# Kernel optimization log

Hardware: AMD Instinct MI355X
Metric: run time of the kernel (lower is better)

Reference implementation:

```python
import jax, jax.numpy as jnp
import numpy as np
import math

B, S, D, E, H = 8, 384, 768, 768, 12
HD = E // H
MAXL = 512

def _xavier(key, shape):
    fan_in, fan_out = shape[1], shape[0]
    lim = math.sqrt(6.0 / (fan_in + fan_out))
    return jax.random.uniform(key, shape, jnp.float32, -lim, lim)

def setup_inputs() -> dict:
    key = jax.random.key(0)
    ks = jax.random.split(key, 12)
    return {
        "x": jax.random.normal(ks[0], (B, S, D), jnp.float32),
        "mask": jnp.ones((B, S), jnp.int32),
        "segment_ids": jax.random.randint(ks[1], (B, S), 0, 2).astype(jnp.int32),
        "sep_distances": jax.random.normal(ks[2], (B, S), jnp.float32),
        "Wq": _xavier(ks[3], (E, D)), "bq": jnp.zeros((E,), jnp.float32),
        "Wk": _xavier(ks[4], (E, D)), "bk": jnp.zeros((E,), jnp.float32),
        "Wv": _xavier(ks[5], (E, D)), "bv": jnp.zeros((E,), jnp.float32),
        "rel_emb": jax.random.normal(ks[6], (2 * MAXL - 1, D), jnp.float32),
        "Wpk": _xavier(ks[7], (E, D)), "bpk": jnp.zeros((E,), jnp.float32),
        "Wpq": _xavier(ks[8], (E, D)), "bpq": jnp.zeros((E,), jnp.float32),
        "same_bias": jnp.zeros((H,), jnp.float32),
        "cross_bias": jnp.zeros((H,), jnp.float32),
        "sep_scale": jnp.full((H,), 0.25, jnp.float32),
        "sep_decay": jnp.full((H,), 0.35, jnp.float32),
        "Wo": _xavier(ks[9], (D, E)), "bo": jnp.zeros((D,), jnp.float32),
    }

def reference(x, mask, segment_ids, sep_distances, Wq, bq, Wk, bk, Wv, bv,
              rel_emb, Wpk, bpk, Wpq, bpq, same_bias, cross_bias,
              sep_scale, sep_decay, Wo, bo):
    b, s, _ = x.shape
    def shape_heads(t):  # [b,s,E] -> [b,H,s,HD]
        return t.reshape(b, s, H, HD).transpose(0, 2, 1, 3)
    q = shape_heads(x @ Wq.T + bq)
    k = shape_heads(x @ Wk.T + bk)
    v = shape_heads(x @ Wv.T + bv)
    # relative positions i - j, clamped and shifted
    rel_pos = jnp.arange(s)[:, None] - jnp.arange(s)[None, :]
    rel_pos = jnp.clip(rel_pos, -(MAXL - 1), MAXL - 1) + (MAXL - 1)
    rel = rel_emb[rel_pos]                     # [s,s,D]
    pos_k = (rel @ Wpk.T + bpk).reshape(s, s, H, HD)  # [i,j,h,d]
    pos_q = (rel @ Wpq.T + bpq).reshape(s, s, H, HD)
    c2c = jnp.einsum('bhid,bhjd->bhij', q, k)
    c2p = jnp.einsum('bhid,ijhd->bhij', q, pos_k)
    p2c = jnp.einsum('ijhd,bhjd->bhij', pos_q, k)
    logits = (c2c + c2p + p2c) / math.sqrt(HD * 3.0)
    # segment bias
    same = (segment_ids[:, :, None] == segment_ids[:, None, :]).astype(jnp.float32)[:, None]  # [b,1,s,s]
    cross = 1.0 - same
    hb = lambda p: p[None, :, None, None]
    seg_bias = same * hb(same_bias) + cross * hb(cross_bias)
    abs_sep = jnp.abs(sep_distances)
    gap = jnp.abs(abs_sep[:, :, None] - abs_sep[:, None, :])[:, None]  # [b,1,s,s]
    decay = jax.nn.softplus(sep_decay)[None, :, None, None] + 1e-4
    seg_bias = seg_bias + cross * jnp.exp(-gap * decay) * hb(sep_scale)
    logits = logits + seg_bias
    # mask: [b,s] -> [b,1,1,s]
    m = mask[:, None, None, :]
    logits = jnp.where(m == 0, jnp.float32(-9e15), logits)
    attn = jax.nn.softmax(logits, axis=-1)
    vals = jnp.einsum('bhij,bhjd->bhid', attn, v)
    vals = vals.transpose(0, 2, 1, 3).reshape(b, s, E)
    return vals @ Wo.T + bo
```

## Files before the change

kernel.cpp:

```cpp
#include <hip/hip_runtime.h>
#include <math.h>

#define B_  8
#define S_  384
#define H_  12
#define HD_ 64
#define E_  768
#define D_  768

typedef float  floatx4 __attribute__((ext_vector_type(4)));
typedef __bf16 bf16x8  __attribute__((ext_vector_type(8)));
typedef unsigned int ux4 __attribute__((ext_vector_type(4)));

__device__ __forceinline__ unsigned short f2bf(float f) {
    union { float f; unsigned u; } x; x.f = f;
    unsigned r = x.u + 0x7fff + ((x.u >> 16) & 1);
    return (unsigned short)(r >> 16);
}
__device__ __forceinline__ float bf2f(unsigned short u) {
    union { unsigned u; float f; } x; x.u = ((unsigned)u) << 16;
    return x.f;
}
__device__ __forceinline__ bf16x8 gld8(const unsigned short* p) {
    return __builtin_bit_cast(bf16x8, *(const ux4*)p);
}
__device__ __forceinline__ int tadr(int row, int cD) {
    return (row * 8 + (cD ^ (row & 7))) * 8;
}
__device__ __forceinline__ bf16x8 lds8(const unsigned short* base, int row, int cD) {
    return __builtin_bit_cast(bf16x8, *(const ux4*)(base + tadr(row, cD)));
}

__global__ __launch_bounds__(256) void convert_all(
    const float* __restrict__ x,
    const float* __restrict__ Wq, const float* __restrict__ Wk,
    const float* __restrict__ Wv, const float* __restrict__ Wo,
    const float* __restrict__ Wpk, const float* __restrict__ Wpq,
    const float* __restrict__ rel128,
    unsigned short* __restrict__ xb,
    unsigned short* __restrict__ wqb, unsigned short* __restrict__ wkb,
    unsigned short* __restrict__ wvb, unsigned short* __restrict__ wob,
    unsigned short* __restrict__ wpkb, unsigned short* __restrict__ wpqb,
    unsigned short* __restrict__ relb)
{
    const int seg = blockIdx.y;
    const int e = (blockIdx.x * 256 + threadIdx.x) * 4;
    const float* src;
    unsigned short* dst;
    if (seg < 4)       { src = x + (size_t)seg * 589824; dst = xb + (size_t)seg * 589824; }
    else if (seg == 4) { src = Wq;  dst = wqb; }
    else if (seg == 5) { src = Wk;  dst = wkb; }
    else if (seg == 6) { src = Wv;  dst = wvb; }
    else if (seg == 7) { src = Wo;  dst = wob; }
    else if (seg == 8) { src = Wpk; dst = wpkb; }
    else if (seg == 9) { src = Wpq; dst = wpqb; }
    else               { src = rel128; dst = relb; }

    float4 v;
    if (seg == 10 && e >= 767 * 768) v = make_float4(0.f, 0.f, 0.f, 0.f);
    else                             v = *(const float4*)(src + e);
    ushort4 o;
    o.x = f2bf(v.x); o.y = f2bf(v.y); o.z = f2bf(v.z); o.w = f2bf(v.w);
    *(ushort4*)(dst + e) = o;
}

__global__ __launch_bounds__(256) void proj_all(
    const unsigned short* __restrict__ xb, const unsigned short* __restrict__ relb,
    const unsigned short* __restrict__ wq, const unsigned short* __restrict__ wk,
    const unsigned short* __restrict__ wv, const unsigned short* __restrict__ wpk,
    const unsigned short* __restrict__ wpq,
    const float* __restrict__ bq, const float* __restrict__ bk,
    const float* __restrict__ bv, const float* __restrict__ bpk,
    const float* __restrict__ bpq,
    unsigned short* __restrict__ qb, unsigned short* __restrict__ kb,
    unsigned short* __restrict__ vtb, unsigned short* __restrict__ pkb,
    unsigned short* __restrict__ pqb)
{
    const int z = blockIdx.z;
    if (z >= 3 && blockIdx.y >= 6) return;

    const unsigned short* A = (z < 3) ? xb : relb;
    const unsigned short* W = (z == 0) ? wq : (z == 1) ? wk : (z == 2) ? wv
                            : (z == 3) ? wpk : wpq;
    const float* bias = (z == 0) ? bq : (z == 1) ? bk : (z == 2) ? bv
                      : (z == 3) ? bpk : bpq;
    unsigned short* C = (z == 0) ? qb : (z == 1) ? kb : (z == 2) ? vtb
                      : (z == 3) ? pkb : pqb;

    __shared__ unsigned short As[128 * 32];
    __shared__ unsigned short Ws[128 * 32];

    const int tid  = threadIdx.x;
    const int lane = tid & 63;
    const int wv_  = tid >> 6;
    const int wy   = wv_ >> 1, wx = wv_ & 1;
    const int quad = lane >> 4, l16 = lane & 15;
    const int m0 = blockIdx.y * 128, n0 = blockIdx.x * 128;

    floatx4 acc[4][4];
#pragma unroll
    for (int i = 0; i < 4; ++i)
#pragma unroll
        for (int j = 0; j < 4; ++j) acc[i][j] = (floatx4){0.f, 0.f, 0.f, 0.f};

    const int koff = quad * 8;

    for (int k0 = 0; k0 < 768; k0 += 32) {
        __syncthreads();
#pragma unroll
        for (int r = 0; r < 2; ++r) {
            int idx = tid + 256 * r;
            int row = idx >> 2, c8 = (idx & 3) * 8;
            const unsigned short* ga = A + (size_t)(m0 + row) * 768 + k0 + c8;
            const unsigned short* gw = W + (size_t)(n0 + row) * 768 + k0 + c8;
            __builtin_amdgcn_global_load_lds(
                (__attribute__((address_space(1))) void*)ga,
                (__attribute__((address_space(3))) void*)&As[idx * 8], 16, 0, 0);
            __builtin_amdgcn_global_load_lds(
                (__attribute__((address_space(1))) void*)gw,
                (__attribute__((address_space(3))) void*)&Ws[idx * 8], 16, 0, 0);
        }
        __syncthreads();

        bf16x8 a[4], b[4];
#pragma unroll
        for (int mi = 0; mi < 4; ++mi)
            a[mi] = __builtin_bit_cast(bf16x8,
                *(const ux4*)&As[(wy * 64 + mi * 16 + l16) * 32 + koff]);
#pragma unroll
        for (int ni = 0; ni < 4; ++ni)
            b[ni] = __builtin_bit_cast(bf16x8,
                *(const ux4*)&Ws[(wx * 64 + ni * 16 + l16) * 32 + koff]);
#pragma unroll
        for (int mi = 0; mi < 4; ++mi)
#pragma unroll
            for (int ni = 0; ni < 4; ++ni)
                acc[mi][ni] = __builtin_amdgcn_mfma_f32_16x16x32_bf16(
                    a[mi], b[ni], acc[mi][ni], 0, 0, 0);
    }

#pragma unroll
    for (int ni = 0; ni < 4; ++ni) {
        const int n = n0 + wx * 64 + ni * 16 + l16;
        const float bn = bias[n];
#pragma unroll
        for (int mi = 0; mi < 4; ++mi) {
            const int mbase = m0 + wy * 64 + mi * 16 + quad * 4;
            if (z == 2) {
                const int bb = mbase / S_, s = mbase - bb * S_;
                const int h = n >> 6, hd = n & 63;
                ushort4 o;
                o.x = f2bf(acc[mi][ni][0] + bn);
                o.y = f2bf(acc[mi][ni][1] + bn);
                o.z = f2bf(acc[mi][ni][2] + bn);
                o.w = f2bf(acc[mi][ni][3] + bn);
                *(ushort4*)&C[(((size_t)(bb * H_ + h) << 6) + hd) * S_ + s] = o;
            } else if (z < 2) {
#pragma unroll
                for (int reg = 0; reg < 4; ++reg) {
                    const int m = mbase + reg;
                    const int bb = m / S_, s = m - bb * S_;
                    const int h = n >> 6, hd = n & 63;
                    C[(((size_t)(bb * H_ + h) * S_ + s) << 6) + hd] =
                        f2bf(acc[mi][ni][reg] + bn);
                }
            } else {
#pragma unroll
                for (int reg = 0; reg < 4; ++reg)
                    C[(size_t)(mbase + reg) * 768 + n] = f2bf(acc[mi][ni][reg] + bn);
            }
        }
    }
}

__global__ __launch_bounds__(256) void gemm_out(
    const unsigned short* __restrict__ A, const unsigned short* __restrict__ W,
    const float* __restrict__ bias, float* __restrict__ C)
{
    __shared__ unsigned short As[128 * 32];
    __shared__ unsigned short Ws[128 * 32];

    const int tid  = threadIdx.x;
    const int lane = tid & 63;
    const int wv_  = tid >> 6;
    const int wy   = wv_ >> 1, wx = wv_ & 1;
    const int quad = lane >> 4, l16 = lane & 15;
    const int m0 = blockIdx.y * 128, n0 = blockIdx.x * 128;

    floatx4 acc[4][4];
#pragma unroll
    for (int i = 0; i < 4; ++i)
#pragma unroll
        for (int j = 0; j < 4; ++j) acc[i][j] = (floatx4){0.f, 0.f, 0.f, 0.f};

    const int koff = quad * 8;

    for (int k0 = 0; k0 < 768; k0 += 32) {
        __syncthreads();
#pragma unroll
        for (int r = 0; r < 2; ++r) {
            int idx = tid + 256 * r;
            int row = idx >> 2, c8 = (idx & 3) * 8;
            const unsigned short* ga = A + (size_t)(m0 + row) * 768 + k0 + c8;
            const unsigned short* gw = W + (size_t)(n0 + row) * 768 + k0 + c8;
            __builtin_amdgcn_global_load_lds(
                (__attribute__((address_space(1))) void*)ga,
                (__attribute__((address_space(3))) void*)&As[idx * 8], 16, 0, 0);
            __builtin_amdgcn_global_load_lds(
                (__attribute__((address_space(1))) void*)gw,
                (__attribute__((address_space(3))) void*)&Ws[idx * 8], 16, 0, 0);
        }
        __syncthreads();

        bf16x8 a[4], b[4];
#pragma unroll
        for (int mi = 0; mi < 4; ++mi)
            a[mi] = __builtin_bit_cast(bf16x8,
                *(const ux4*)&As[(wy * 64 + mi * 16 + l16) * 32 + koff]);
#pragma unroll
        for (int ni = 0; ni < 4; ++ni)
            b[ni] = __builtin_bit_cast(bf16x8,
                *(const ux4*)&Ws[(wx * 64 + ni * 16 + l16) * 32 + koff]);
#pragma unroll
        for (int mi = 0; mi < 4; ++mi)
#pragma unroll
            for (int ni = 0; ni < 4; ++ni)
                acc[mi][ni] = __builtin_amdgcn_mfma_f32_16x16x32_bf16(
                    a[mi], b[ni], acc[mi][ni], 0, 0, 0);
    }

#pragma unroll
    for (int ni = 0; ni < 4; ++ni) {
        const int n = n0 + wx * 64 + ni * 16 + l16;
        const float bn = bias[n];
#pragma unroll
        for (int mi = 0; mi < 4; ++mi)
#pragma unroll
            for (int reg = 0; reg < 4; ++reg) {
                const int m = m0 + wy * 64 + mi * 16 + quad * 4 + reg;
                C[(size_t)m * 768 + n] = acc[mi][ni][reg] + bn;
            }
    }
}

__global__ __launch_bounds__(256) void attn_mfma(
    const unsigned short* __restrict__ qg, const unsigned short* __restrict__ kg,
    const unsigned short* __restrict__ vtg,
    const unsigned short* __restrict__ pkg, const unsigned short* __restrict__ pqg,
    const int* __restrict__ seg, const float* __restrict__ sep,
    const int* __restrict__ mask,
    const float* __restrict__ same_bias, const float* __restrict__ cross_bias,
    const float* __restrict__ sep_scale, const float* __restrict__ sep_decay,
    unsigned short* __restrict__ part_O, float* __restrict__ part_ml)
{
    __shared__ unsigned short Ks [64 * 64];
    __shared__ unsigned short Vts[64 * 64];
    __shared__ unsigned short PKs[128 * 64];
    __shared__ unsigned short PQs[128 * 64];
    __shared__ float CP[64 * 68];

    const int tid  = threadIdx.x;
    const int lane = tid & 63, w = tid >> 6;
    const int l16  = lane & 15, quad = lane >> 4;
    const int ty = tid >> 4, tx = tid & 15;
    const int it = blockIdx.x, h = blockIdx.y;
    const int b  = blockIdx.z / 6, jt = blockIdx.z - 6 * b;
    const int i0 = it * 64, j0 = jt * 64;
    const size_t bh = (size_t)(b * H_ + h);

    const unsigned short* kbase  = kg  + bh * S_ * 64;
    const unsigned short* vtbase = vtg + bh * 64 * S_;
    const int dbase = i0 - j0 + 320;

    bf16x8 qf[2];
#pragma unroll
    for (int ks = 0; ks < 2; ++ks)
        qf[ks] = gld8(qg + (bh * S_ + i0 + 16 * w + l16) * 64 + ks * 32 + quad * 8);

#pragma unroll
    for (int r = 0; r < 2; ++r) {
        const int idx = tid + 256 * r;
        const int row = idx >> 3, cL = idx & 7;
        const int cD = cL ^ (row & 7);
        __builtin_amdgcn_global_load_lds(
            (__attribute__((address_space(1))) void*)(kbase + (size_t)(j0 + row) * 64 + cD * 8),
            (__attribute__((address_space(3))) void*)&Ks[idx * 8], 16, 0, 0);
        __builtin_amdgcn_global_load_lds(
            (__attribute__((address_space(1))) void*)(vtbase + (size_t)row * S_ + j0 + cD * 8),
            (__attribute__((address_space(3))) void*)&Vts[idx * 8], 16, 0, 0);
    }
#pragma unroll
    for (int r = 0; r < 4; ++r) {
        const int idx = tid + 256 * r;
        const int row = idx >> 3, cL = idx & 7;
        const int cD = cL ^ (row & 7);
        const size_t go = (size_t)(dbase + row) * 768 + h * 64 + cD * 8;
        __builtin_amdgcn_global_load_lds(
            (__attribute__((address_space(1))) void*)(pkg + go),
            (__attribute__((address_space(3))) void*)&PKs[idx * 8], 16, 0, 0);
        __builtin_amdgcn_global_load_lds(
            (__attribute__((address_space(1))) void*)(pqg + go),
            (__attribute__((address_space(3))) void*)&PQs[idx * 8], 16, 0, 0);
    }

    float ai_r[4]; int si_r[4];
#pragma unroll
    for (int p = 0; p < 4; ++p) {
        const int ii = 4 * ty + p;
        ai_r[p] = fabsf(sep[b * S_ + i0 + ii]);
        si_r[p] = seg[b * S_ + i0 + ii];
    }

    const float sb  = same_bias[h];
    const float cb  = cross_bias[h];
    const float ssc = sep_scale[h];
    const float sd  = sep_decay[h];
    const float dec = fmaxf(sd, 0.f) + log1pf(__expf(-fabsf(sd))) + 1e-4f;
    const float isc = 0.07216878364870323f;

    __syncthreads();

    bf16x8 kf[4][2];
#pragma unroll
    for (int nj = 0; nj < 4; ++nj)
#pragma unroll
        for (int ks = 0; ks < 2; ++ks)
            kf[nj][ks] = lds8(Ks, 16 * nj + l16, ks * 4 + quad);

#pragma unroll
    for (int nj = 0; nj < 4; ++nj) {
        floatx4 acc = (floatx4){0.f, 0.f, 0.f, 0.f};
#pragma unroll
        for (int ks = 0; ks < 2; ++ks)
            acc = __builtin_amdgcn_mfma_f32_16x16x32_bf16(qf[ks], kf[nj][ks], acc, 0, 0, 0);
#pragma unroll
        for (int reg = 0; reg < 4; ++reg) {
            const int ii = 16 * w + quad * 4 + reg;
            CP[ii * 68 + 16 * nj + l16] = acc[reg];
        }
    }

#pragma unroll
    for (int f = 0; f < 5; ++f) {
        const int nd = w + f;
        floatx4 acc = (floatx4){0.f, 0.f, 0.f, 0.f};
#pragma unroll
        for (int ks = 0; ks < 2; ++ks) {
            bf16x8 bf = lds8(PKs, 16 * nd + l16, ks * 4 + quad);
            acc = __builtin_amdgcn_mfma_f32_16x16x32_bf16(qf[ks], bf, acc, 0, 0, 0);
        }
        const int ddloc = 16 * nd + l16;
#pragma unroll
        for (int reg = 0; reg < 4; ++reg) {
            const int ii = 16 * w + quad * 4 + reg;
            const int jj = ii - ddloc + 63;
            if (jj >= 0 && jj < 64)
                CP[ii * 68 + jj] += acc[reg];
        }
    }

#pragma unroll
    for (int f = 0; f < 5; ++f) {
        const int nd = w + f;
        bf16x8 pqf[2];
#pragma unroll
        for (int ks = 0; ks < 2; ++ks)
            pqf[ks] = lds8(PQs, 16 * nd + l16, ks * 4 + quad);
#pragma unroll
        for (int g = 0; g < 2; ++g) {
            const int nj = (g == 0) ? (3 - f) : (4 - f);
            if (nj < 0 || nj > 3) continue;
            floatx4 acc = (floatx4){0.f, 0.f, 0.f, 0.f};
#pragma unroll
            for (int ks = 0; ks < 2; ++ks)
                acc = __builtin_amdgcn_mfma_f32_16x16x32_bf16(pqf[ks], kf[nj][ks], acc, 0, 0, 0);
            const int jj = 16 * nj + l16;
#pragma unroll
            for (int reg = 0; reg < 4; ++reg) {
                const int ddloc = 16 * nd + quad * 4 + reg;
                const int ii = ddloc + jj - 63;
                if (ii >= 16 * w && ii < 16 * w + 16)
                    CP[ii * 68 + jj] += acc[reg];
            }
        }
    }

    unsigned short* Pp = (unsigned short*)CP;
    float* pml = part_ml + (size_t)(jt * 576 + ((b * H_ + h) * 6 + it)) * 128;
#pragma unroll
    for (int p = 0; p < 4; ++p) {
        const int ii = 4 * ty + p;
        const float aii = ai_r[p];
        const int   sii = si_r[p];
        float lg[4];
        float tmax = -INFINITY;
#pragma unroll
        for (int r = 0; r < 4; ++r) {
            const int jl = 4 * tx + r;
            float xv = CP[ii * 68 + jl] * isc;
            const float ajv = fabsf(sep[b * S_ + j0 + jl]);
            const int   sjv = seg[b * S_ + j0 + jl];
            const float gap = fabsf(aii - ajv);
            const float bias = (sii == sjv) ? sb
                             : cb + __expf(-gap * dec) * ssc;
            xv += bias;
            if (mask[b * S_ + j0 + jl] == 0) xv = -9.0e15f;
            lg[r] = xv;
            tmax = fmaxf(tmax, xv);
        }
#pragma unroll
        for (int off = 1; off < 16; off <<= 1)
            tmax = fmaxf(tmax, __shfl_xor(tmax, off));
        float rs = 0.f;
        ushort4 pw;
#pragma unroll
        for (int r = 0; r < 4; ++r) {
            const float e = __expf(lg[r] - tmax);
            rs += e;
            ((unsigned short*)&pw)[r] = f2bf(e);
        }
#pragma unroll
        for (int off = 1; off < 16; off <<= 1)
            rs += __shfl_xor(rs, off);
        if (tx == 0) {
            pml[ii]      = tmax;
            pml[64 + ii] = rs;
        }
        *(ushort4*)&Pp[ii * 136 + 4 * tx] = pw;
    }

    bf16x8 pA[2];
#pragma unroll
    for (int ks = 0; ks < 2; ++ks)
        pA[ks] = __builtin_bit_cast(bf16x8,
            *(const ux4*)&Pp[(16 * w + l16) * 136 + ks * 32 + quad * 8]);
    floatx4 O[4];
#pragma unroll
    for (int nd = 0; nd < 4; ++nd) {
        O[nd] = (floatx4){0.f, 0.f, 0.f, 0.f};
#pragma unroll
        for (int ks = 0; ks < 2; ++ks) {
            bf16x8 bf = lds8(Vts, 16 * nd + l16, ks * 4 + quad);
            O[nd] = __builtin_amdgcn_mfma_f32_16x16x32_bf16(pA[ks], bf, O[nd], 0, 0, 0);
        }
    }

    unsigned short* pO = part_O + (size_t)(jt * 576 + ((b * H_ + h) * 6 + it)) * 4096;
#pragma unroll
    for (int nd = 0; nd < 4; ++nd) {
        const int d = 16 * nd + l16;
#pragma unroll
        for (int reg = 0; reg < 4; ++reg) {
            const int ii = 16 * w + quad * 4 + reg;
            pO[ii * 64 + d] = f2bf(O[nd][reg]);
        }
    }
}

__global__ __launch_bounds__(256) void merge_attn(
    const unsigned short* __restrict__ part_O, const float* __restrict__ part_ml,
    unsigned short* __restrict__ vals)
{
    const int idx = blockIdx.x;
    const int b  = idx / (H_ * 6);
    const int r  = idx - b * H_ * 6;
    const int h  = r / 6, it = r - h * 6;
    const int tid = threadIdx.x;
    const int ii = tid >> 2, c = (tid & 3) * 16;

    float m[6], l[6];
#pragma unroll
    for (int jc = 0; jc < 6; ++jc) {
        const float* pml = part_ml + (size_t)(jc * 576 + idx) * 128;
        m[jc] = pml[ii];
        l[jc] = pml[64 + ii];
    }
    float M = m[0];
#pragma unroll
    for (int jc = 1; jc < 6; ++jc) M = fmaxf(M, m[jc]);
    float wsum = 0.f, wc[6];
#pragma unroll
    for (int jc = 0; jc < 6; ++jc) {
        wc[jc] = __expf(m[jc] - M);
        wsum += wc[jc] * l[jc];
    }
    const float inv = (wsum > 0.f) ? 1.f / wsum : 0.f;

    float o[16];
#pragma unroll
    for (int e = 0; e < 16; ++e) o[e] = 0.f;
#pragma unroll
    for (int jc = 0; jc < 6; ++jc) {
        const unsigned short* pO = part_O + ((size_t)(jc * 576 + idx)) * 4096
                                 + ii * 64 + c;
        ux4 u0 = *(const ux4*)pO;
        ux4 u1 = *(const ux4*)(pO + 8);
        const unsigned short* us0 = (const unsigned short*)&u0;
        const unsigned short* us1 = (const unsigned short*)&u1;
#pragma unroll
        for (int e = 0; e < 8; ++e) {
            o[e]     += wc[jc] * bf2f(us0[e]);
            o[8 + e] += wc[jc] * bf2f(us1[e]);
        }
    }
    ushort4 w0, w1, w2, w3;
#pragma unroll
    for (int e = 0; e < 4; ++e) {
        ((unsigned short*)&w0)[e] = f2bf(o[e] * inv);
        ((unsigned short*)&w1)[e] = f2bf(o[4 + e] * inv);
        ((unsigned short*)&w2)[e] = f2bf(o[8 + e] * inv);
        ((unsigned short*)&w3)[e] = f2bf(o[12 + e] * inv);
    }
    unsigned short* dst = vals + ((size_t)(b * S_ + it * 64 + ii)) * E_ + h * 64 + c;
    *(ushort4*)(dst)      = w0;
    *(ushort4*)(dst + 4)  = w1;
    *(ushort4*)(dst + 8)  = w2;
    *(ushort4*)(dst + 12) = w3;
}

extern "C" void kernel_launch(void* const* d_in, const int* in_sizes, int n_in,
                              void* d_out, int out_size, void* d_ws, size_t ws_size,
                              hipStream_t stream)
{
    const float* x         = (const float*)d_in[0];
    const int*   mask      = (const int*)d_in[1];
    const int*   seg       = (const int*)d_in[2];
    const float* sep       = (const float*)d_in[3];
    const float* Wq        = (const float*)d_in[4];
    const float* bq        = (const float*)d_in[5];
    const float* Wk        = (const float*)d_in[6];
    const float* bk        = (const float*)d_in[7];
    const float* Wv        = (const float*)d_in[8];
    const float* bv        = (const float*)d_in[9];
    const float* rel_emb   = (const float*)d_in[10];
    const float* Wpk       = (const float*)d_in[11];
    const float* bpk       = (const float*)d_in[12];
    const float* Wpq       = (const float*)d_in[13];
    const float* bpq       = (const float*)d_in[14];
    const float* same_bias = (const float*)d_in[15];
    const float* cross_bias= (const float*)d_in[16];
    const float* sep_scale = (const float*)d_in[17];
    const float* sep_decay = (const float*)d_in[18];
    const float* Wo        = (const float*)d_in[19];
    const float* bo        = (const float*)d_in[20];

    const size_t QKVN = (size_t)B_ * S_ * E_;
    const size_t WN   = (size_t)768 * 768;

    unsigned short* xb    = (unsigned short*)d_ws;
    unsigned short* wqb   = xb   + QKVN;
    unsigned short* wkb   = wqb  + WN;
    unsigned short* wvb   = wkb  + WN;
    unsigned short* wob   = wvb  + WN;
    unsigned short* wpkb  = wob  + WN;
    unsigned short* wpqb  = wpkb + WN;
    unsigned short* relb  = wpqb + WN;
    unsigned short* qb    = relb + WN;
    unsigned short* kb    = qb   + QKVN;
    unsigned short* vtb   = kb   + QKVN;
    unsigned short* pkb   = vtb  + QKVN;
    unsigned short* pqb   = pkb  + WN;
    unsigned short* valsb = pqb  + WN;
    unsigned short* partO = valsb + QKVN;
    float*          partml= (float*)(partO + (size_t)6 * 576 * 4096);

    convert_all<<<dim3(576, 11), 256, 0, stream>>>(
        x, Wq, Wk, Wv, Wo, Wpk, Wpq, rel_emb + (size_t)128 * D_,
        xb, wqb, wkb, wvb, wob, wpkb, wpqb, relb);

    proj_all<<<dim3(6, 24, 5), 256, 0, stream>>>(
        xb, relb, wqb, wkb, wvb, wpkb, wpqb,
        bq, bk, bv, bpk, bpq, qb, kb, vtb, pkb, pqb);

    attn_mfma<<<dim3(6, 12, 48), 256, 0, stream>>>(
        qb, kb, vtb, pkb, pqb, seg, sep, mask,
        same_bias, cross_bias, sep_scale, sep_decay, partO, partml);

    merge_attn<<<dim3(576), 256, 0, stream>>>(partO, partml, valsb);

    gemm_out<<<dim3(6, 24), 256, 0, stream>>>(valsb, wob, bo, (float*)d_out);
}
```

Baseline: 238.4 us.

## Load K/V fragments directly to registers and split positional logits into bf16 buffers

K and V^T MFMA fragments are now read from global memory straight into registers instead of being staged through LDS, which removes those LDS tiles and the LDS fragment reads. The c2p and p2c results are no longer accumulated with read-modify-write into the fp32 CP tile. They are written as bf16 into two separate padded LDS buffers and summed with the c2c scores when the softmax reads them. This removes the serialized LDS read-modify-write traffic. The cost is more register pressure, less coalesced global loads, and bf16 rounding of the positional terms before the softmax.

```diff
diff --git a/kernel.cpp b/kernel.cpp
--- a/kernel.cpp
+++ b/kernel.cpp
@@ -253,11 +253,11 @@
     const float* __restrict__ sep_scale, const float* __restrict__ sep_decay,
     unsigned short* __restrict__ part_O, float* __restrict__ part_ml)
 {
-    __shared__ unsigned short Ks [64 * 64];
-    __shared__ unsigned short Vts[64 * 64];
     __shared__ unsigned short PKs[128 * 64];
     __shared__ unsigned short PQs[128 * 64];
     __shared__ float CP[64 * 68];
+    __shared__ unsigned short C2Ps[64 * 72];
+    __shared__ unsigned short P2Cs[64 * 72];
 
     const int tid  = threadIdx.x;
     const int lane = tid & 63, w = tid >> 6;
@@ -272,23 +272,6 @@
     const unsigned short* vtbase = vtg + bh * 64 * S_;
     const int dbase = i0 - j0 + 320;
 
-    bf16x8 qf[2];
-#pragma unroll
-    for (int ks = 0; ks < 2; ++ks)
-        qf[ks] = gld8(qg + (bh * S_ + i0 + 16 * w + l16) * 64 + ks * 32 + quad * 8);
-
-#pragma unroll
-    for (int r = 0; r < 2; ++r) {
-        const int idx = tid + 256 * r;
-        const int row = idx >> 3, cL = idx & 7;
-        const int cD = cL ^ (row & 7);
-        __builtin_amdgcn_global_load_lds(
-            (__attribute__((address_space(1))) void*)(kbase + (size_t)(j0 + row) * 64 + cD * 8),
-            (__attribute__((address_space(3))) void*)&Ks[idx * 8], 16, 0, 0);
-        __builtin_amdgcn_global_load_lds(
-            (__attribute__((address_space(1))) void*)(vtbase + (size_t)row * S_ + j0 + cD * 8),
-            (__attribute__((address_space(3))) void*)&Vts[idx * 8], 16, 0, 0);
-    }
 #pragma unroll
     for (int r = 0; r < 4; ++r) {
         const int idx = tid + 256 * r;
@@ -303,6 +286,25 @@
             (__attribute__((address_space(3))) void*)&PQs[idx * 8], 16, 0, 0);
     }
 
+    bf16x8 qf[2];
+#pragma unroll
+    for (int ks = 0; ks < 2; ++ks)
+        qf[ks] = gld8(qg + (bh * S_ + i0 + 16 * w + l16) * 64 + ks * 32 + quad * 8);
+
+    bf16x8 kf[4][2];
+#pragma unroll
+    for (int nj = 0; nj < 4; ++nj)
+#pragma unroll
+        for (int ks = 0; ks < 2; ++ks)
+            kf[nj][ks] = gld8(kbase + (size_t)(j0 + 16 * nj + l16) * 64 + ks * 32 + quad * 8);
+
+    bf16x8 vtf[4][2];
+#pragma unroll
+    for (int nd = 0; nd < 4; ++nd)
+#pragma unroll
+        for (int ks = 0; ks < 2; ++ks)
+            vtf[nd][ks] = gld8(vtbase + (size_t)(16 * nd + l16) * S_ + j0 + ks * 32 + quad * 8);
+
     float ai_r[4]; int si_r[4];
 #pragma unroll
     for (int p = 0; p < 4; ++p) {
@@ -320,13 +322,6 @@
 
     __syncthreads();
 
-    bf16x8 kf[4][2];
-#pragma unroll
-    for (int nj = 0; nj < 4; ++nj)
-#pragma unroll
-        for (int ks = 0; ks < 2; ++ks)
-            kf[nj][ks] = lds8(Ks, 16 * nj + l16, ks * 4 + quad);
-
 #pragma unroll
     for (int nj = 0; nj < 4; ++nj) {
         floatx4 acc = (floatx4){0.f, 0.f, 0.f, 0.f};
@@ -355,7 +350,7 @@
             const int ii = 16 * w + quad * 4 + reg;
             const int jj = ii - ddloc + 63;
             if (jj >= 0 && jj < 64)
-                CP[ii * 68 + jj] += acc[reg];
+                C2Ps[ii * 72 + jj] = f2bf(acc[reg]);
         }
     }
 
@@ -380,7 +375,7 @@
                 const int ddloc = 16 * nd + quad * 4 + reg;
                 const int ii = ddloc + jj - 63;
                 if (ii >= 16 * w && ii < 16 * w + 16)
-                    CP[ii * 68 + jj] += acc[reg];
+                    P2Cs[ii * 72 + jj] = f2bf(acc[reg]);
             }
         }
     }
@@ -392,12 +387,19 @@
         const int ii = 4 * ty + p;
         const float aii = ai_r[p];
         const int   sii = si_r[p];
+        const float4 cc = *(const float4*)&CP[ii * 68 + 4 * tx];
+        const ushort4 u1 = *(const ushort4*)&C2Ps[ii * 72 + 4 * tx];
+        const ushort4 u2 = *(const ushort4*)&P2Cs[ii * 72 + 4 * tx];
         float lg[4];
+        lg[0] = cc.x + bf2f(u1.x) + bf2f(u2.x);
+        lg[1] = cc.y + bf2f(u1.y) + bf2f(u2.y);
+        lg[2] = cc.z + bf2f(u1.z) + bf2f(u2.z);
+        lg[3] = cc.w + bf2f(u1.w) + bf2f(u2.w);
         float tmax = -INFINITY;
 #pragma unroll
         for (int r = 0; r < 4; ++r) {
             const int jl = 4 * tx + r;
-            float xv = CP[ii * 68 + jl] * isc;
+            float xv = lg[r] * isc;
             const float ajv = fabsf(sep[b * S_ + j0 + jl]);
             const int   sjv = seg[b * S_ + j0 + jl];
             const float gap = fabsf(aii - ajv);
@@ -439,10 +441,8 @@
     for (int nd = 0; nd < 4; ++nd) {
         O[nd] = (floatx4){0.f, 0.f, 0.f, 0.f};
 #pragma unroll
-        for (int ks = 0; ks < 2; ++ks) {
-            bf16x8 bf = lds8(Vts, 16 * nd + l16, ks * 4 + quad);
-            O[nd] = __builtin_amdgcn_mfma_f32_16x16x32_bf16(pA[ks], bf, O[nd], 0, 0, 0);
-        }
+        for (int ks = 0; ks < 2; ++ks)
+            O[nd] = __builtin_amdgcn_mfma_f32_16x16x32_bf16(pA[ks], vtf[nd][ks], O[nd], 0, 0, 0);
     }
 
     unsigned short* pO = part_O + (size_t)(jt * 576 + ((b * H_ + h) * 6 + it)) * 4096;
```

Result: slower. 244.6 us (+2.6%).

## Retile projection and output GEMMs to 64x128 tiles with K=64 and swizzled LDS

Applied to the files above, without the earlier changes.

The projection and output GEMMs move from 128x128 tiles with K-step 32 to 64x128 tiles with K-step 64. LDS chunks get an XOR swizzle so MFMA operand reads avoid bank conflicts. The projection launch becomes a flat 1D grid that skips the empty rel-projection blocks. Smaller tiles give more blocks and better fill on 256 CUs, at the cost of less operand reuse per block and fewer MFMAs per wave.

```diff
diff --git a/kernel.cpp b/kernel.cpp
--- a/kernel.cpp
+++ b/kernel.cpp
@@ -76,8 +76,15 @@
     unsigned short* __restrict__ vtb, unsigned short* __restrict__ pkb,
     unsigned short* __restrict__ pqb)
 {
-    const int z = blockIdx.z;
-    if (z >= 3 && blockIdx.y >= 6) return;
+    const int bid = blockIdx.x;
+    int z, mt, nt;
+    if (bid < 864) {
+        z = bid / 288; const int r = bid - z * 288; mt = r / 6; nt = r - mt * 6;
+    } else {
+        const int r2 = bid - 864; z = 3 + r2 / 72;
+        const int r = r2 % 72; mt = r / 6; nt = r - mt * 6;
+    }
+    const int m0 = mt * 64, n0 = nt * 128;
 
     const unsigned short* A = (z < 3) ? xb : relb;
     const unsigned short* W = (z == 0) ? wq : (z == 1) ? wk : (z == 2) ? wv
@@ -87,65 +94,68 @@
     unsigned short* C = (z == 0) ? qb : (z == 1) ? kb : (z == 2) ? vtb
                       : (z == 3) ? pkb : pqb;
 
-    __shared__ unsigned short As[128 * 32];
-    __shared__ unsigned short Ws[128 * 32];
+    __shared__ unsigned short As[64 * 64];
+    __shared__ unsigned short Ws[128 * 64];
 
     const int tid  = threadIdx.x;
     const int lane = tid & 63;
     const int wv_  = tid >> 6;
-    const int wy   = wv_ >> 1, wx = wv_ & 1;
     const int quad = lane >> 4, l16 = lane & 15;
-    const int m0 = blockIdx.y * 128, n0 = blockIdx.x * 128;
-
-    floatx4 acc[4][4];
+
+    floatx4 acc[4][2];
 #pragma unroll
     for (int i = 0; i < 4; ++i)
 #pragma unroll
-        for (int j = 0; j < 4; ++j) acc[i][j] = (floatx4){0.f, 0.f, 0.f, 0.f};
-
-    const int koff = quad * 8;
-
-    for (int k0 = 0; k0 < 768; k0 += 32) {
+        for (int j = 0; j < 2; ++j) acc[i][j] = (floatx4){0.f, 0.f, 0.f, 0.f};
+
+    for (int k0 = 0; k0 < 768; k0 += 64) {
         __syncthreads();
 #pragma unroll
         for (int r = 0; r < 2; ++r) {
-            int idx = tid + 256 * r;
-            int row = idx >> 2, c8 = (idx & 3) * 8;
-            const unsigned short* ga = A + (size_t)(m0 + row) * 768 + k0 + c8;
-            const unsigned short* gw = W + (size_t)(n0 + row) * 768 + k0 + c8;
+            const int idx = tid + 256 * r;
+            const int row = idx >> 3, cL = idx & 7, cD = cL ^ (row & 7);
             __builtin_amdgcn_global_load_lds(
-                (__attribute__((address_space(1))) void*)ga,
+                (__attribute__((address_space(1))) void*)(A + (size_t)(m0 + row) * 768 + k0 + cD * 8),
                 (__attribute__((address_space(3))) void*)&As[idx * 8], 16, 0, 0);
+        }
+#pragma unroll
+        for (int r = 0; r < 4; ++r) {
+            const int idx = tid + 256 * r;
+            const int row = idx >> 3, cL = idx & 7, cD = cL ^ (row & 7);
             __builtin_amdgcn_global_load_lds(
-                (__attribute__((address_space(1))) void*)gw,
+                (__attribute__((address_space(1))) void*)(W + (size_t)(n0 + row) * 768 + k0 + cD * 8),
                 (__attribute__((address_space(3))) void*)&Ws[idx * 8], 16, 0, 0);
         }
         __syncthreads();
 
-        bf16x8 a[4], b[4];
+        bf16x8 a[4][2], b[2][2];
 #pragma unroll
         for (int mi = 0; mi < 4; ++mi)
-            a[mi] = __builtin_bit_cast(bf16x8,
-                *(const ux4*)&As[(wy * 64 + mi * 16 + l16) * 32 + koff]);
-#pragma unroll
-        for (int ni = 0; ni < 4; ++ni)
-            b[ni] = __builtin_bit_cast(bf16x8,
-                *(const ux4*)&Ws[(wx * 64 + ni * 16 + l16) * 32 + koff]);
+#pragma unroll
+            for (int kc = 0; kc < 2; ++kc)
+                a[mi][kc] = lds8(As, mi * 16 + l16, kc * 4 + quad);
+#pragma unroll
+        for (int ni = 0; ni < 2; ++ni)
+#pragma unroll
+            for (int kc = 0; kc < 2; ++kc)
+                b[ni][kc] = lds8(Ws, wv_ * 32 + ni * 16 + l16, kc * 4 + quad);
 #pragma unroll
         for (int mi = 0; mi < 4; ++mi)
 #pragma unroll
-            for (int ni = 0; ni < 4; ++ni)
-                acc[mi][ni] = __builtin_amdgcn_mfma_f32_16x16x32_bf16(
-                    a[mi], b[ni], acc[mi][ni], 0, 0, 0);
-    }
-
-#pragma unroll
-    for (int ni = 0; ni < 4; ++ni) {
-        const int n = n0 + wx * 64 + ni * 16 + l16;
+            for (int ni = 0; ni < 2; ++ni)
+#pragma unroll
+                for (int kc = 0; kc < 2; ++kc)
+                    acc[mi][ni] = __builtin_amdgcn_mfma_f32_16x16x32_bf16(
+                        a[mi][kc], b[ni][kc], acc[mi][ni], 0, 0, 0);
+    }
+
+#pragma unroll
+    for (int ni = 0; ni < 2; ++ni) {
+        const int n = n0 + wv_ * 32 + ni * 16 + l16;
         const float bn = bias[n];
 #pragma unroll
         for (int mi = 0; mi < 4; ++mi) {
-            const int mbase = m0 + wy * 64 + mi * 16 + quad * 4;
+            const int mbase = m0 + mi * 16 + quad * 4;
             if (z == 2) {
                 const int bb = mbase / S_, s = mbase - bb * S_;
                 const int h = n >> 6, hd = n & 63;
@@ -177,67 +187,73 @@
     const unsigned short* __restrict__ A, const unsigned short* __restrict__ W,
     const float* __restrict__ bias, float* __restrict__ C)
 {
-    __shared__ unsigned short As[128 * 32];
-    __shared__ unsigned short Ws[128 * 32];
+    const int mt = blockIdx.x / 6, nt = blockIdx.x - mt * 6;
+    const int m0 = mt * 64, n0 = nt * 128;
+
+    __shared__ unsigned short As[64 * 64];
+    __shared__ unsigned short Ws[128 * 64];
 
     const int tid  = threadIdx.x;
     const int lane = tid & 63;
     const int wv_  = tid >> 6;
-    const int wy   = wv_ >> 1, wx = wv_ & 1;
     const int quad = lane >> 4, l16 = lane & 15;
-    const int m0 = blockIdx.y * 128, n0 = blockIdx.x * 128;
-
-    floatx4 acc[4][4];
+
+    floatx4 acc[4][2];
 #pragma unroll
     for (int i = 0; i < 4; ++i)
 #pragma unroll
-        for (int j = 0; j < 4; ++j) acc[i][j] = (floatx4){0.f, 0.f, 0.f, 0.f};
-
-    const int koff = quad * 8;
-
-    for (int k0 = 0; k0 < 768; k0 += 32) {
+        for (int j = 0; j < 2; ++j) acc[i][j] = (floatx4){0.f, 0.f, 0.f, 0.f};
+
+    for (int k0 = 0; k0 < 768; k0 += 64) {
         __syncthreads();
 #pragma unroll
         for (int r = 0; r < 2; ++r) {
-            int idx = tid + 256 * r;
-            int row = idx >> 2, c8 = (idx & 3) * 8;
-            const unsigned short* ga = A + (size_t)(m0 + row) * 768 + k0 + c8;
-            const unsigned short* gw = W + (size_t)(n0 + row) * 768 + k0 + c8;
+            const int idx = tid + 256 * r;
+            const int row = idx >> 3, cL = idx & 7, cD = cL ^ (row & 7);
             __builtin_amdgcn_global_load_lds(
-                (__attribute__((address_space(1))) void*)ga,
+                (__attribute__((address_space(1))) void*)(A + (size_t)(m0 + row) * 768 + k0 + cD * 8),
                 (__attribute__((address_space(3))) void*)&As[idx * 8], 16, 0, 0);
+        }
+#pragma unroll
+        for (int r = 0; r < 4; ++r) {
+            const int idx = tid + 256 * r;
+            const int row = idx >> 3, cL = idx & 7, cD = cL ^ (row & 7);
             __builtin_amdgcn_global_load_lds(
-                (__attribute__((address_space(1))) void*)gw,
+                (__attribute__((address_space(1))) void*)(W + (size_t)(n0 + row) * 768 + k0 + cD * 8),
                 (__attribute__((address_space(3))) void*)&Ws[idx * 8], 16, 0, 0);
         }
         __syncthreads();
 
-        bf16x8 a[4], b[4];
+        bf16x8 a[4][2], b[2][2];
 #pragma unroll
         for (int mi = 0; mi < 4; ++mi)
-            a[mi] = __builtin_bit_cast(bf16x8,
-                *(const ux4*)&As[(wy * 64 + mi * 16 + l16) * 32 + koff]);
-#pragma unroll
-        for (int ni = 0; ni < 4; ++ni)
-            b[ni] = __builtin_bit_cast(bf16x8,
-                *(const ux4*)&Ws[(wx * 64 + ni * 16 + l16) * 32 + koff]);
+#pragma unroll
+            for (int kc = 0; kc < 2; ++kc)
+                a[mi][kc] = lds8(As, mi * 16 + l16, kc * 4 + quad);
+#pragma unroll
+        for (int ni = 0; ni < 2; ++ni)
+#pragma unroll
+            for (int kc = 0; kc < 2; ++kc)
+                b[ni][kc] = lds8(Ws, wv_ * 32 + ni * 16 + l16, kc * 4 + quad);
 #pragma unroll
         for (int mi = 0; mi < 4; ++mi)
 #pragma unroll
-            for (int ni = 0; ni < 4; ++ni)
-                acc[mi][ni] = __builtin_amdgcn_mfma_f32_16x16x32_bf16(
-                    a[mi], b[ni], acc[mi][ni], 0, 0, 0);
-    }
-
-#pragma unroll
-    for (int ni = 0; ni < 4; ++ni) {
-        const int n = n0 + wx * 64 + ni * 16 + l16;
+            for (int ni = 0; ni < 2; ++ni)
+#pragma unroll
+                for (int kc = 0; kc < 2; ++kc)
+                    acc[mi][ni] = __builtin_amdgcn_mfma_f32_16x16x32_bf16(
+                        a[mi][kc], b[ni][kc], acc[mi][ni], 0, 0, 0);
+    }
+
+#pragma unroll
+    for (int ni = 0; ni < 2; ++ni) {
+        const int n = n0 + wv_ * 32 + ni * 16 + l16;
         const float bn = bias[n];
 #pragma unroll
         for (int mi = 0; mi < 4; ++mi)
 #pragma unroll
             for (int reg = 0; reg < 4; ++reg) {
-                const int m = m0 + wy * 64 + mi * 16 + quad * 4 + reg;
+                const int m = m0 + mi * 16 + quad * 4 + reg;
                 C[(size_t)m * 768 + n] = acc[mi][ni][reg] + bn;
             }
     }
@@ -568,7 +584,7 @@
         x, Wq, Wk, Wv, Wo, Wpk, Wpq, rel_emb + (size_t)128 * D_,
         xb, wqb, wkb, wvb, wob, wpkb, wpqb, relb);
 
-    proj_all<<<dim3(6, 24, 5), 256, 0, stream>>>(
+    proj_all<<<dim3(1008), 256, 0, stream>>>(
         xb, relb, wqb, wkb, wvb, wpkb, wpqb,
         bq, bk, bv, bpk, bpq, qb, kb, vtb, pkb, pqb);
 
@@ -578,5 +594,5 @@
 
     merge_attn<<<dim3(576), 256, 0, stream>>>(partO, partml, valsb);
 
-    gemm_out<<<dim3(6, 24), 256, 0, stream>>>(valsb, wob, bo, (float*)d_out);
-}
+    gemm_out<<<dim3(288), 256, 0, stream>>>(valsb, wob, bo, (float*)d_out);
+}
```

Measured after the change: 212.6 us. 1.12x faster.
